# Performance work log

Hardware: AMD Instinct MI355X
Metric: run time of the kernel (lower is better)

Reference implementation:

```python
import jax, jax.numpy as jnp
import numpy as np

B, N, C = 4, 2048, 1024


def setup_inputs() -> dict:
    key = jax.random.key(0)
    ks = jax.random.split(key, 5)
    s = 1.0 / np.sqrt(C)
    return {
        "event_f": jax.random.normal(ks[0], (B, N, C), dtype=jnp.float32),
        "img_f": jax.random.normal(ks[1], (B, N, C), dtype=jnp.float32),
        "Wq": jax.random.normal(ks[2], (C, C), dtype=jnp.float32) * s,
        "bq": jnp.zeros((C,), dtype=jnp.float32),
        "Wk": jax.random.normal(ks[3], (C, C), dtype=jnp.float32) * s,
        "bk": jnp.zeros((C,), dtype=jnp.float32),
        "Wv": jax.random.normal(ks[4], (C, C), dtype=jnp.float32) * s,
        "bv": jnp.zeros((C,), dtype=jnp.float32),
    }


def reference(event_f, img_f, Wq, bq, Wk, bk, Wv, bv):
    # pointwise projections (conv_query/key/val as 1x1 / Linear C->C)
    q = jnp.einsum("bnc,cd->bnd", event_f, Wq) + bq  # [B,N,C]
    k = jnp.einsum("bnc,cd->bnd", img_f, Wk) + bk
    v = jnp.einsum("bnc,cd->bnd", img_f, Wv) + bv
    scale = 1.0 / jnp.sqrt(jnp.asarray(q.shape[-1], dtype=q.dtype))
    scores = jnp.einsum("bqc,bkc->bqk", q, k) * scale  # [B,N,N]
    p_attn = jax.nn.softmax(scores, axis=-1)
    return jnp.einsum("bqk,bkc->bqc", p_attn, v)  # [B,N,C]
```

## Files before the change

kernel.cpp:

```cpp
#include <hip/hip_runtime.h>
#include <hip/hip_bf16.h>
#include <stdint.h>

typedef __bf16 bf16;
typedef __attribute__((ext_vector_type(8))) __bf16 bf16x8;
typedef __attribute__((ext_vector_type(4))) __bf16 bf16x4;
typedef __attribute__((ext_vector_type(4))) float f32x4;

typedef __attribute__((address_space(3))) char* lds_ptr;
typedef const __attribute__((address_space(1))) char* glb_ptr;

#define BZ 4
#define NN 2048
#define CC 1024

__device__ __forceinline__ void gload_lds16(const bf16* g, bf16* l) {
    __builtin_amdgcn_global_load_lds((glb_ptr)g, (lds_ptr)l, 16, 0, 0);
}

__device__ __forceinline__ void bar() {
    asm volatile("" ::: "memory");
    __builtin_amdgcn_s_barrier();
    asm volatile("" ::: "memory");
}

__global__ void ucomp(const float* __restrict__ Wk, const float* __restrict__ bq,
                      float* __restrict__ u) {
    __shared__ float red[4];
    const int c = blockIdx.x, t = threadIdx.x;
    float p = 0.f;
    for (int d = t; d < CC; d += 256) p += Wk[(size_t)c * CC + d] * bq[d];
#pragma unroll
    for (int off = 32; off; off >>= 1) p += __shfl_xor(p, off);
    if ((t & 63) == 0) red[t >> 6] = p;
    __syncthreads();
    if (t == 0) u[c] = red[0] + red[1] + red[2] + red[3];
}

__global__ void cvt4(const float* __restrict__ e, const float* __restrict__ im,
                     const float* __restrict__ wq, const float* __restrict__ wk,
                     bf16* __restrict__ oe, bf16* __restrict__ oi,
                     bf16* __restrict__ owq, bf16* __restrict__ owk,
                     const float* __restrict__ u, float* __restrict__ beta,
                     int n8, int w8) {
    int idx = blockIdx.x * blockDim.x + threadIdx.x;
    const float* src;
    bf16* dst;
    int j;
    bool isI = false;
    if (idx < n8) { src = e; dst = oe; j = idx; }
    else if (idx < 2 * n8) { src = im; dst = oi; j = idx - n8; isI = true; }
    else if (idx < 2 * n8 + w8) { src = wq; dst = owq; j = idx - 2 * n8; }
    else if (idx < 2 * n8 + 2 * w8) { src = wk; dst = owk; j = idx - 2 * n8 - w8; }
    else return;
    float4 x = ((const float4*)src)[2 * j], y = ((const float4*)src)[2 * j + 1];
    bf16x8 o;
    o[0] = (bf16)x.x; o[1] = (bf16)x.y; o[2] = (bf16)x.z; o[3] = (bf16)x.w;
    o[4] = (bf16)y.x; o[5] = (bf16)y.y; o[6] = (bf16)y.z; o[7] = (bf16)y.w;
    *(bf16x8*)(dst + 8 * (size_t)j) = o;
    if (isI) {
        int c0 = (j & 127) * 8;
        float p = x.x * u[c0] + x.y * u[c0 + 1] + x.z * u[c0 + 2] + x.w * u[c0 + 3] +
                  y.x * u[c0 + 4] + y.y * u[c0 + 5] + y.z * u[c0 + 6] + y.w * u[c0 + 7];
#pragma unroll
        for (int off = 32; off; off >>= 1) p += __shfl_xor(p, off);
        if ((threadIdx.x & 63) == 0) atomicAdd(&beta[j >> 7], p);
    }
}

__global__ void transposeW1(const float* __restrict__ W, bf16* __restrict__ Wt) {
    __shared__ bf16 t[32][33];
    int d0 = blockIdx.x * 32, c0 = blockIdx.y * 32;
    int tx = threadIdx.x, ty = threadIdx.y;
#pragma unroll
    for (int i = 0; i < 4; i++)
        t[ty + 8 * i][tx] = (bf16)W[(size_t)(c0 + ty + 8 * i) * CC + d0 + tx];
    __syncthreads();
#pragma unroll
    for (int i = 0; i < 4; i++)
        Wt[(size_t)(d0 + ty + 8 * i) * CC + c0 + tx] = t[tx][ty + 8 * i];
}

__global__ void sumcvt(const float* __restrict__ P, bf16* __restrict__ G, int n4) {
    int i = blockIdx.x * blockDim.x + threadIdx.x;
    if (i >= n4) return;
    const size_t S1 = (size_t)CC * CC;
    float4 a = ((const float4*)P)[i];
    float4 b = ((const float4*)(P + S1))[i];
    float4 c = ((const float4*)(P + 2 * S1))[i];
    float4 d = ((const float4*)(P + 3 * S1))[i];
    bf16x4 o;
    o[0] = (bf16)(a.x + b.x + c.x + d.x);
    o[1] = (bf16)(a.y + b.y + c.y + d.y);
    o[2] = (bf16)(a.z + b.z + c.z + d.z);
    o[3] = (bf16)(a.w + b.w + c.w + d.w);
    *(bf16x4*)(G + 4 * (size_t)i) = o;
}


#define STAGE_A(kt_, hh_)                                                          \
    do {                                                                           \
        int _kt = (kt_);                                                           \
        if (_kt < nkt) {                                                           \
            const bf16* _s = gAs + (size_t)((hh_) * (BM / 2)) * lda +              \
                             (size_t)_kt * 64;                                     \
            bf16* _d = &LA[_kt & 1][((hh_) * (BM / 2) + wid * 16) * 64];           \
            gload_lds16(_s, _d);                                                   \
            gload_lds16(_s + (size_t)8 * lda, _d + 8 * 64);                        \
        }                                                                          \
    } while (0)

#define STAGE_B(kt_, hh_)                                                          \
    do {                                                                           \
        int _kt = (kt_);                                                           \
        if (_kt < nkt) {                                                           \
            const bf16* _s = gBs + (size_t)((hh_) * (BN / 2)) * ldb +              \
                             (size_t)_kt * 64;                                     \
            bf16* _d = &LB[_kt & 1][((hh_) * (BN / 2) + wid * 16) * 64];           \
            gload_lds16(_s, _d);                                                   \
            gload_lds16(_s + (size_t)8 * ldb, _d + 8 * 64);                        \
        }                                                                          \
    } while (0)

#define LDA_FRAG(buf_, mh_)                                                      \
    do {                                                                         \
        _Pragma("unroll") for (int _i = 0; _i < MI; ++_i)                        \
            _Pragma("unroll") for (int _ks = 0; _ks < 2; ++_ks)                  \
                a[_i][_ks] = *(const bf16x8*)&LA[buf_][                          \
                    (wm + (mh_) * (WAVE_M / 2) + _i * 16 + fr) * 64 +            \
                    (((_ks * 4 + hi) ^ lo) * 8)];                                \
    } while (0)

#define LDB_FRAG(buf_, nh_, dst_)                                                \
    do {                                                                         \
        _Pragma("unroll") for (int _j = 0; _j < 2; ++_j)                         \
            _Pragma("unroll") for (int _ks = 0; _ks < 2; ++_ks)                  \
                dst_[_j][_ks] = *(const bf16x8*)&LB[buf_][                       \
                    (wn + (nh_)*32 + _j * 16 + fr) * 64 +                        \
                    (((_ks * 4 + hi) ^ lo) * 8)];                                \
    } while (0)

#define MMQ(mh_, nh_, b_)                                                        \
    do {                                                                         \
        __builtin_amdgcn_s_setprio(1);                                           \
        _Pragma("unroll") for (int _i = 0; _i < MI; ++_i)                        \
            _Pragma("unroll") for (int _j = 0; _j < 2; ++_j)                     \
                _Pragma("unroll") for (int _ks = 0; _ks < 2; ++_ks)              \
                    acc[(mh_)*MI + _i][(nh_)*2 + _j] =                           \
                        __builtin_amdgcn_mfma_f32_16x16x32_bf16(                 \
                            a[_i][_ks], b_[_j][_ks],                             \
                            acc[(mh_)*MI + _i][(nh_)*2 + _j], 0, 0, 0);          \
        __builtin_amdgcn_s_setprio(0);                                           \
    } while (0)

#define VMW(n_) asm volatile("s_waitcnt vmcnt(" #n_ ")" ::: "memory")

template <int TB, int BM, int BN, int EPI, bool OUT_F32>
__global__ __launch_bounds__(TB, 2) void gemm8(
    const bf16* __restrict__ A, int lda,
    const bf16* __restrict__ Bt, int ldb,
    void* __restrict__ Cout, int ldc,
    float* __restrict__ aux, long long sAux,
    const float* __restrict__ fold, long long sFold, float scale,
    long long sA, long long sB, long long sC, int nkt) {
    constexpr int WNW = (TB == 512) ? 4 : 2;
    constexpr int WAVE_M = BM / 2;
    constexpr int MI = WAVE_M / 32;
    static_assert(BN / WNW == 64, "wave_n must be 64");
    __shared__ __align__(16) bf16 LA[2][BM * 64];
    __shared__ __align__(16) bf16 LB[2][BN * 64];

    const int nx = gridDim.x, ny = gridDim.y;
    const int nwg = nx * ny * gridDim.z;
    const int orig = blockIdx.x + nx * (blockIdx.y + ny * blockIdx.z);
    const int q = nwg >> 3, r = nwg & 7;
    const int xcd = orig & 7, land = orig >> 3;
    const int swz = (xcd < r ? xcd * (q + 1) : r * (q + 1) + (xcd - r) * q) + land;
    const int bx = swz % nx;
    const int tmp = swz / nx;
    const int by = tmp % ny, bz = tmp / ny;

    A += (size_t)bz * sA;
    Bt += (size_t)bz * sB;
    const int m0 = by * BM, n0 = bx * BN;
    const int t = threadIdx.x, wid = t >> 6, lane = t & 63;
    const int wm = (wid / WNW) * WAVE_M, wn = (wid % WNW) * 64;
    const int fr = lane & 15, hi = lane >> 4, lo = lane & 7;
    f32x4 acc[2 * MI][4] = {};

    const int srow = lane >> 3;
    const int schunk = lo ^ srow;
    const bf16* gAs = A + (size_t)(m0 + wid * 16 + srow) * lda + schunk * 8;
    const bf16* gBs = Bt + (size_t)(n0 + wid * 16 + srow) * ldb + schunk * 8;

    STAGE_A(0, 0); STAGE_A(0, 1); STAGE_B(0, 0); STAGE_B(0, 1);
    STAGE_B(1, 0); STAGE_A(1, 0); STAGE_B(1, 1);
    VMW(6);
    bar();

    bf16x8 a[MI][2], b0[2][2], b1[2][2];
    for (int kt = 0; kt < nkt; ++kt) {
        const int buf = kt & 1;
        LDA_FRAG(buf, 0);
        LDB_FRAG(buf, 0, b0);
        STAGE_A(kt + 1, 1);
        MMQ(0, 0, b0);
        bar();
        LDB_FRAG(buf, 1, b1);
        MMQ(0, 1, b1);
        bar();
        LDA_FRAG(buf, 1);
        STAGE_B(kt + 2, 0);
        MMQ(1, 1, b1);
        bar();
        STAGE_A(kt + 2, 0);
        STAGE_B(kt + 2, 1);
        MMQ(1, 0, b0);
        if (kt + 2 < nkt) VMW(6);
        else VMW(0);
        bar();
    }

    const int rq = hi * 4;
#pragma unroll
    for (int mh = 0; mh < 2; mh++)
#pragma unroll
        for (int i = 0; i < MI; i++) {
            const int row = m0 + wm + mh * (WAVE_M / 2) + i * 16 + rq;
            float rsum[4] = {0.f, 0.f, 0.f, 0.f};
            float inv[4];
            if (EPI == 4) {
#pragma unroll
                for (int rr = 0; rr < 4; rr++)
                    inv[rr] = 1.f / aux[bz * sAux + row + rr];
            }
#pragma unroll
            for (int nh = 0; nh < 2; nh++)
#pragma unroll
                for (int j = 0; j < 2; j++) {
                    int col = n0 + wn + nh * 32 + j * 16 + fr;
                    float fc = (EPI == 5) ? fold[bz * sFold + col] * scale : 0.f;
                    f32x4 v = acc[mh * MI + i][nh * 2 + j];
#pragma unroll
                    for (int rr = 0; rr < 4; rr++) {
                        float o = v[rr] * scale;
                        if (EPI == 2) o += aux[row + rr];
                        if (EPI == 5) { o = __expf(o + fc - 6.f); rsum[rr] += o; }
                        if (EPI == 4) o *= inv[rr];
                        if (OUT_F32)
                            ((float*)Cout)[(size_t)bz * sC + (size_t)(row + rr) * ldc + col] = o;
                        else
                            ((bf16*)Cout)[(size_t)bz * sC + (size_t)(row + rr) * ldc + col] = (bf16)o;
                    }
                }
            if (EPI == 5) {
#pragma unroll
                for (int rr = 0; rr < 4; rr++) {
                    float s = rsum[rr];
                    s += __shfl_xor(s, 1);
                    s += __shfl_xor(s, 2);
                    s += __shfl_xor(s, 4);
                    s += __shfl_xor(s, 8);
                    if (fr == 0) atomicAdd(&aux[bz * sAux + row + rr], s);
                }
            }
        }
}

extern "C" void kernel_launch(void* const* d_in, const int* in_sizes, int n_in,
                              void* d_out, int out_size, void* d_ws, size_t ws_size,
                              hipStream_t stream) {
    const float* event_f = (const float*)d_in[0];
    const float* img_f   = (const float*)d_in[1];
    const float* Wq = (const float*)d_in[2];
    const float* bq = (const float*)d_in[3];
    const float* Wk = (const float*)d_in[4];
    const float* bk = (const float*)d_in[5];
    const float* Wv = (const float*)d_in[6];
    const float* bv = (const float*)d_in[7];
    float* out = (float*)d_out;
    (void)bk;

    bf16* ws = (bf16*)d_ws;
    const size_t MC = (size_t)BZ * NN * CC;
    const size_t CCsq = (size_t)CC * CC;
    bf16* Ebf  = ws;
    bf16* Ibf  = ws + MC;
    size_t off = 2 * MC;
    bf16* Wqbf = ws + off; off += CCsq;
    bf16* Wkbf = ws + off; off += CCsq;
    bf16* Wvt  = ws + off; off += CCsq;
    bf16* Gt   = ws + off; off += CCsq;
    bf16* Tb   = ws + off; off += MC;
    bf16* VT   = ws + off; off += MC;
    bf16* S    = ws + off; off += 2 * MC;
    float* Gpart = (float*)S;
    float* fbase  = (float*)(ws + off);
    float* rowsum = fbase;
    float* beta   = fbase + BZ * NN;
    float* u      = fbase + 2 * BZ * NN;

    hipMemsetAsync(rowsum, 0, 2 * BZ * NN * sizeof(float), stream);
    ucomp<<<dim3(CC), dim3(256), 0, stream>>>(Wk, bq, u);
    {
        int n8 = (int)(MC / 8), w8 = (int)(CCsq / 8);
        int tot = 2 * n8 + 2 * w8;
        cvt4<<<dim3((tot + 255) / 256), dim3(256), 0, stream>>>(
            event_f, img_f, Wq, Wk, Ebf, Ibf, Wqbf, Wkbf, u, beta, n8, w8);
    }
    transposeW1<<<dim3(CC / 32, CC / 32), dim3(32, 8), 0, stream>>>(Wv, Wvt);
    gemm8<256, 128, 128, 0, true><<<dim3(8, 8, 4), dim3(256), 0, stream>>>(
        Wkbf, CC, Wqbf, CC, Gpart, CC, nullptr, 0, nullptr, 0, 1.f,
        256, 256, (long long)CCsq, 4);
    sumcvt<<<dim3((CCsq / 4 + 255) / 256), dim3(256), 0, stream>>>(
        Gpart, Gt, (int)(CCsq / 4));
    gemm8<256, 128, 128, 0, false><<<dim3(CC / 128, (BZ * NN) / 128, 1), dim3(256), 0, stream>>>(
        Ebf, CC, Gt, CC, Tb, CC, nullptr, 0, nullptr, 0, 1.f, 0, 0, 0, CC / 64);
    gemm8<256, 128, 128, 2, false><<<dim3(NN / 128, CC / 128, BZ), dim3(256), 0, stream>>>(
        Wvt, CC, Ibf, CC, VT, NN, (float*)bv, 0, nullptr, 0, 1.f,
        0, (long long)NN * CC, (long long)CC * NN, CC / 64);
    gemm8<512, 256, 256, 5, false><<<dim3(NN / 256, NN / 256, BZ), dim3(512), 0, stream>>>(
        Tb, CC, Ibf, CC, S, NN, rowsum, NN, beta, NN, 1.f / 32.f,
        (long long)NN * CC, (long long)NN * CC, (long long)NN * NN, CC / 64);
    gemm8<256, 128, 128, 4, true><<<dim3(CC / 128, NN / 128, BZ), dim3(256), 0, stream>>>(
        S, NN, VT, NN, out, CC, rowsum, NN, nullptr, 0, 1.f,
        (long long)NN * NN, (long long)CC * NN, (long long)NN * CC, NN / 64);
}
```

Before: 168.9 us.

## Restructure 256-thread GEMM main loop with fewer barriers and fold memset into ucomp

For the 256-thread GEMM instantiations, all A and B fragments of a k-tile are now loaded from LDS up front into separate registers, and the four MFMA quadrants run with two barriers per iteration instead of four. The hipMemsetAsync that zeroes rowsum/beta is removed, and the zeroing is done inside the ucomp kernel, saving one launch. The cost is higher register pressure from holding both A halves at once, which could lower occupancy under the 2-blocks launch bound. The 512-thread path keeps the original schedule.

Result: faster. 160.1 us (-5.2%).

```diff
diff --git a/kernel.cpp b/kernel.cpp
--- a/kernel.cpp
+++ b/kernel.cpp
@@ -25,9 +25,11 @@
 }
 
 __global__ void ucomp(const float* __restrict__ Wk, const float* __restrict__ bq,
-                      float* __restrict__ u) {
+                      float* __restrict__ u, float* __restrict__ zbuf) {
     __shared__ float red[4];
     const int c = blockIdx.x, t = threadIdx.x;
+    int gid = blockIdx.x * 256 + t;
+    if (gid < 2 * BZ * NN) zbuf[gid] = 0.f;
     float p = 0.f;
     for (int d = t; d < CC; d += 256) p += Wk[(size_t)c * CC + d] * bq[d];
 #pragma unroll
@@ -122,11 +124,11 @@
         }                                                                          \
     } while (0)
 
-#define LDA_FRAG(buf_, mh_)                                                      \
+#define LDA_FRAG(buf_, mh_, dst_)                                                \
     do {                                                                         \
         _Pragma("unroll") for (int _i = 0; _i < MI; ++_i)                        \
             _Pragma("unroll") for (int _ks = 0; _ks < 2; ++_ks)                  \
-                a[_i][_ks] = *(const bf16x8*)&LA[buf_][                          \
+                dst_[_i][_ks] = *(const bf16x8*)&LA[buf_][                       \
                     (wm + (mh_) * (WAVE_M / 2) + _i * 16 + fr) * 64 +            \
                     (((_ks * 4 + hi) ^ lo) * 8)];                                \
     } while (0)
@@ -140,7 +142,7 @@
                     (((_ks * 4 + hi) ^ lo) * 8)];                                \
     } while (0)
 
-#define MMQ(mh_, nh_, b_)                                                        \
+#define MMQ(mh_, nh_, a_, b_)                                                    \
     do {                                                                         \
         __builtin_amdgcn_s_setprio(1);                                           \
         _Pragma("unroll") for (int _i = 0; _i < MI; ++_i)                        \
@@ -148,7 +150,7 @@
                 _Pragma("unroll") for (int _ks = 0; _ks < 2; ++_ks)              \
                     acc[(mh_)*MI + _i][(nh_)*2 + _j] =                           \
                         __builtin_amdgcn_mfma_f32_16x16x32_bf16(                 \
-                            a[_i][_ks], b_[_j][_ks],                             \
+                            a_[_i][_ks], b_[_j][_ks],                            \
                             acc[(mh_)*MI + _i][(nh_)*2 + _j], 0, 0, 0);          \
         __builtin_amdgcn_s_setprio(0);                                           \
     } while (0)
@@ -198,27 +200,49 @@
     VMW(6);
     bar();
 
-    bf16x8 a[MI][2], b0[2][2], b1[2][2];
-    for (int kt = 0; kt < nkt; ++kt) {
-        const int buf = kt & 1;
-        LDA_FRAG(buf, 0);
-        LDB_FRAG(buf, 0, b0);
-        STAGE_A(kt + 1, 1);
-        MMQ(0, 0, b0);
-        bar();
-        LDB_FRAG(buf, 1, b1);
-        MMQ(0, 1, b1);
-        bar();
-        LDA_FRAG(buf, 1);
-        STAGE_B(kt + 2, 0);
-        MMQ(1, 1, b1);
-        bar();
-        STAGE_A(kt + 2, 0);
-        STAGE_B(kt + 2, 1);
-        MMQ(1, 0, b0);
-        if (kt + 2 < nkt) VMW(6);
-        else VMW(0);
-        bar();
+    bf16x8 aA[MI][2], aB[MI][2], b0[2][2], b1[2][2];
+    if constexpr (TB == 256) {
+        for (int kt = 0; kt < nkt; ++kt) {
+            const int buf = kt & 1;
+            LDA_FRAG(buf, 0, aA);
+            LDA_FRAG(buf, 1, aB);
+            LDB_FRAG(buf, 0, b0);
+            LDB_FRAG(buf, 1, b1);
+            STAGE_A(kt + 1, 1);
+            MMQ(0, 0, aA, b0);
+            MMQ(0, 1, aA, b1);
+            bar();
+            STAGE_B(kt + 2, 0);
+            STAGE_B(kt + 2, 1);
+            STAGE_A(kt + 2, 0);
+            MMQ(1, 1, aB, b1);
+            MMQ(1, 0, aB, b0);
+            if (kt + 2 < nkt) VMW(6);
+            else VMW(0);
+            bar();
+        }
+    } else {
+        for (int kt = 0; kt < nkt; ++kt) {
+            const int buf = kt & 1;
+            LDA_FRAG(buf, 0, aA);
+            LDB_FRAG(buf, 0, b0);
+            STAGE_A(kt + 1, 1);
+            MMQ(0, 0, aA, b0);
+            bar();
+            LDB_FRAG(buf, 1, b1);
+            MMQ(0, 1, aA, b1);
+            bar();
+            LDA_FRAG(buf, 1, aB);
+            STAGE_B(kt + 2, 0);
+            MMQ(1, 1, aB, b1);
+            bar();
+            STAGE_A(kt + 2, 0);
+            STAGE_B(kt + 2, 1);
+            MMQ(1, 0, aB, b0);
+            if (kt + 2 < nkt) VMW(6);
+            else VMW(0);
+            bar();
+        }
     }
 
     const int rq = hi * 4;
@@ -300,8 +324,7 @@
     float* beta   = fbase + BZ * NN;
     float* u      = fbase + 2 * BZ * NN;
 
-    hipMemsetAsync(rowsum, 0, 2 * BZ * NN * sizeof(float), stream);
-    ucomp<<<dim3(CC), dim3(256), 0, stream>>>(Wk, bq, u);
+    ucomp<<<dim3(CC), dim3(256), 0, stream>>>(Wk, bq, u, rowsum);
     {
         int n8 = (int)(MC / 8), w8 = (int)(CCsq / 8);
         int tot = 2 * n8 + 2 * w8;
```
